# Kernel optimization log

Measured on AMD Instinct MI355X. Metric: run time of the kernel, lower is better.

## Reference

```python
import jax, jax.numpy as jnp
import numpy as np

D_MODEL = 1024
NUM_TILES = 8
BATCH = 4096
TEMPERATURE = 0.5

gelu = lambda x: jax.nn.gelu(x, approximate=False)  # torch nn.GELU default = exact erf


def setup_inputs() -> dict:
    key = jax.random.key(0)
    ks = jax.random.split(key, 12)
    d, t = D_MODEL, NUM_TILES
    s = lambda fan_in: 1.0 / np.sqrt(fan_in)
    return {
        "x": jax.random.normal(ks[0], (BATCH, d), jnp.float32),
        # router: Linear(d,d) -> GELU -> Linear(d,num_tiles); weights stored (in,out)
        "Wr1": jax.random.uniform(ks[1], (d, d), jnp.float32, -s(d), s(d)),
        "br1": jax.random.uniform(ks[2], (d,), jnp.float32, -s(d), s(d)),
        "Wr2": jax.random.uniform(ks[3], (d, t), jnp.float32, -s(d), s(d)),
        "br2": jax.random.uniform(ks[4], (t,), jnp.float32, -s(d), s(d)),
        # tile nets: Linear(d,2d) -> GELU -> Linear(2d,d), stacked over tiles
        "W1": jax.random.uniform(ks[5], (t, d, 2 * d), jnp.float32, -s(d), s(d)),
        "b1": jax.random.uniform(ks[6], (t, 2 * d), jnp.float32, -s(d), s(d)),
        "W2": jax.random.uniform(ks[7], (t, 2 * d, d), jnp.float32, -s(2 * d), s(2 * d)),
        "b2": jax.random.uniform(ks[8], (t, d), jnp.float32, -s(2 * d), s(2 * d)),
        # output projection Linear(d,d)
        "Wo": jax.random.uniform(ks[9], (d, d), jnp.float32, -s(d), s(d)),
        "bo": jax.random.uniform(ks[10], (d,), jnp.float32, -s(d), s(d)),
    }


def reference(x, Wr1, br1, Wr2, br2, W1, b1, W2, b2, Wo, bo):
    # router logits / temperature
    route_logits = (gelu(x @ Wr1 + br1) @ Wr2 + br2) / TEMPERATURE  # (B, T)
    tile_idx = jnp.argmax(route_logits, axis=-1)                    # (B,)

    # hard routing: compute all tile MLPs, then select the argmax tile per token
    # (dense equivalent of per-sample dispatch; same math as the torch loop)
    h = gelu(jnp.einsum("bd,tdf->btf", x, W1) + b1[None])           # (B, T, 2d)
    tile_out = jnp.einsum("btf,tfd->btd", h, W2) + b2[None]         # (B, T, d)
    selected = jnp.take_along_axis(tile_out, tile_idx[:, None, None], axis=1)[:, 0]  # (B, d)

    output = selected @ Wo + bo                                     # (B, d)
    return output, tile_idx, route_logits
```

## Files before the change

### kernel.cpp

```cpp
#include <hip/hip_runtime.h>
#include <hip/hip_bf16.h>
#include <math.h>
#include <stdint.h>

typedef __bf16 bf16_t;
typedef __bf16 bf16x8 __attribute__((ext_vector_type(8)));
typedef float  f32x4  __attribute__((ext_vector_type(4)));

#define BATCH   4096
#define DM      1024
#define DFF     2048
#define NTILES  8
#define MAXXB   40

__device__ __forceinline__ float gelu_exact(float x) {
    return 0.5f * x * (1.0f + erff(x * 0.70710678118654752440f));
}

__device__ __forceinline__ void async_ld16(const bf16_t* g, bf16_t* l) {
    __builtin_amdgcn_global_load_lds(
        (const __attribute__((address_space(1))) void*)g,
        (__attribute__((address_space(3))) void*)l, 16, 0, 0);
}

__device__ __forceinline__ f32x4 mfma16(bf16x8 a, bf16x8 b, f32x4 c) {
    return __builtin_amdgcn_mfma_f32_16x16x32_bf16(a, b, c, 0, 0, 0);
}

template<bool LO>
__device__ void tconv64_body(const float* __restrict__ src, bf16_t* __restrict__ outh,
                             bf16_t* __restrict__ outl, int K, int N, int kt, int nt,
                             float4* t , int tid) {
    const int k0 = kt * 64, n0 = nt * 64;
#pragma unroll
    for (int p = 0; p < 4; ++p) {
        int row = p * 16 + (tid >> 4);
        int c = tid & 15;
        float4 v = *(const float4*)(src + (size_t)(k0 + row) * N + n0 + c * 4);
        t[row * 16 + (c ^ ((row >> 2) & 15))] = v;
    }
    __syncthreads();
    const int n = tid >> 2, b = tid & 3;
    const float* tf = (const float*)t;
    float v[16];
#pragma unroll
    for (int i = 0; i < 16; ++i) {
        int k = 16 * b + i;
        int f4 = k * 16 + ((n >> 2) ^ ((k >> 2) & 15));
        v[i] = tf[f4 * 4 + (n & 3)];
    }
    bf16x8 h0, h1;
#pragma unroll
    for (int i = 0; i < 8; ++i) { h0[i] = (bf16_t)v[i]; h1[i] = (bf16_t)v[8 + i]; }
    size_t oi = (size_t)(n0 + n) * K + k0 + 16 * b;
    *(bf16x8*)(outh + oi) = h0;
    *(bf16x8*)(outh + oi + 8) = h1;
    if constexpr (LO) {
        bf16x8 l0, l1;
#pragma unroll
        for (int i = 0; i < 8; ++i) {
            l0[i] = (bf16_t)(v[i] - (float)h0[i]);
            l1[i] = (bf16_t)(v[8 + i] - (float)h1[i]);
        }
        *(bf16x8*)(outl + oi) = l0;
        *(bf16x8*)(outl + oi + 8) = l1;
    }
}

#define NCVT2 2048
#define PREP_A_GRID (NCVT2 + 256)

__global__ __launch_bounds__(256) void prep_a_kernel(
    const float* __restrict__ x, const float* __restrict__ Wr1,
    bf16_t* __restrict__ xh, bf16_t* __restrict__ xl,
    bf16_t* __restrict__ Wr1h, bf16_t* __restrict__ Wr1l) {
    __shared__ float4 t[64 * 16];
    int b = blockIdx.x;
    if (b < NCVT2) {
        size_t i = (size_t)b * 256 + threadIdx.x;
        const float4* x4 = (const float4*)x;
        float4 v0 = x4[2 * i], v1 = x4[2 * i + 1];
        float f[8] = {v0.x, v0.y, v0.z, v0.w, v1.x, v1.y, v1.z, v1.w};
        bf16x8 h, l;
#pragma unroll
        for (int j = 0; j < 8; ++j) { h[j] = (bf16_t)f[j]; l[j] = (bf16_t)(f[j] - (float)h[j]); }
        *(bf16x8*)(xh + i * 8) = h;
        *(bf16x8*)(xl + i * 8) = l;
        return;
    }
    b -= NCVT2;
    tconv64_body<true>(Wr1, Wr1h, Wr1l, DM, DM, b >> 4, b & 15, t, threadIdx.x);
}

template<bool SPLIT, bool GATHER, bool GELU, bool SCATTER, bool OUTF32, int BK>
__device__ __forceinline__ void gemm_body(
    const bf16_t* __restrict__ A, const bf16_t* __restrict__ Alo,
    const bf16_t* __restrict__ Bt, const bf16_t* __restrict__ Btlo,
    const float* __restrict__ bias,
    float* __restrict__ outF, bf16_t* __restrict__ outB,
    const int* __restrict__ perm, const int* __restrict__ counts,
    int M, int N, int K, int bx, int by,
    bf16_t* As, bf16_t* Bs, bf16_t* Asl, bf16_t* Bsl) {
    constexpr int NCH = BK / 32;
    constexpr int CH  = 128 * 32;
    constexpr int BUF = NCH * CH;

    int tile = 0, rb, cnt = M;
    const int* permT = nullptr;
    if constexpr (GATHER) {
        int xb = bx, t = 0, c = 0;
        while (t < NTILES) {
            c = counts[t];
            int nbk = (c + 127) >> 7;
            if (xb < nbk) break;
            xb -= nbk; ++t;
        }
        if (t == NTILES) return;
        tile = t;
        rb = xb * 128;
        cnt = c;
        permT = perm + tile * BATCH;
    } else {
        rb = bx * 128;
    }
    Bt   += (size_t)tile * K * N;
    if constexpr (SPLIT) Btlo += (size_t)tile * K * N;
    bias += (size_t)tile * N;

    const int lane = threadIdx.x & 63;
    const int wave = threadIdx.x >> 6;
    const int wm = wave & 1, wn = wave >> 1;
    const int nb = by * 128;

    const int srow = lane >> 2;
    const int scol = ((lane & 3) ^ (srow & 3)) * 8;
    const int row = wave * 16 + srow;
    int arow;
    if constexpr (GATHER) {
        int pos = rb + row;
        if (pos > cnt - 1) pos = cnt - 1;
        arow = permT[pos];
    } else {
        arow = rb + row;
    }
    const size_t aoff = (size_t)arow * K + scol;
    const size_t boff = (size_t)(nb + row) * K + scol;

    f32x4 acc[4][2];
#pragma unroll
    for (int i = 0; i < 4; ++i)
#pragma unroll
        for (int j = 0; j < 2; ++j) acc[i][j] = (f32x4){0.f, 0.f, 0.f, 0.f};

    const int lr = lane & 15, lq = lane >> 4;
    const int rdoff = (lr * 4 + (lq ^ (lr & 3))) * 8;

    auto stage = [&](int k0, int buf) {
#pragma unroll
        for (int c = 0; c < NCH; ++c) {
            async_ld16(A  + aoff + k0 + c * 32, &As[buf * BUF + c * CH + wave * 512]);
            async_ld16(Bt + boff + k0 + c * 32, &Bs[buf * BUF + c * CH + wave * 512]);
            if constexpr (SPLIT) {
                async_ld16(Alo  + aoff + k0 + c * 32, &Asl[buf * BUF + c * CH + wave * 512]);
                async_ld16(Btlo + boff + k0 + c * 32, &Bsl[buf * BUF + c * CH + wave * 512]);
            }
        }
    };

    auto compute = [&](int cur) {
#pragma unroll
        for (int kk = 0; kk < NCH; ++kk) {
            const int base = cur * BUF + kk * CH;
            bf16x8 af[4], bfr[2], afl[4], bfl[2];
#pragma unroll
            for (int i = 0; i < 4; ++i) {
                af[i] = *(const bf16x8*)&As[base + (wm * 4 + i) * 512 + rdoff];
                if constexpr (SPLIT)
                    afl[i] = *(const bf16x8*)&Asl[base + (wm * 4 + i) * 512 + rdoff];
            }
#pragma unroll
            for (int j = 0; j < 2; ++j) {
                bfr[j] = *(const bf16x8*)&Bs[base + (wn * 2 + j) * 512 + rdoff];
                if constexpr (SPLIT)
                    bfl[j] = *(const bf16x8*)&Bsl[base + (wn * 2 + j) * 512 + rdoff];
            }
#pragma unroll
            for (int i = 0; i < 4; ++i)
#pragma unroll
                for (int j = 0; j < 2; ++j) {
                    acc[i][j] = mfma16(af[i], bfr[j], acc[i][j]);
                    if constexpr (SPLIT) {
                        acc[i][j] = mfma16(af[i], bfl[j], acc[i][j]);
                        acc[i][j] = mfma16(afl[i], bfr[j], acc[i][j]);
                    }
                }
        }
    };

    stage(0, 0);
    int cur = 0;
    for (int k0 = 0; k0 < K; k0 += BK, cur ^= 1) {
        __syncthreads();
        if (k0 + BK < K) stage(k0 + BK, cur ^ 1);
        compute(cur);
    }

#pragma unroll
    for (int i = 0; i < 4; ++i) {
#pragma unroll
        for (int j = 0; j < 2; ++j) {
#pragma unroll
            for (int r = 0; r < 4; ++r) {
                int m = wm * 64 + i * 16 + lq * 4 + r;
                int n = wn * 32 + j * 16 + lr;
                int pos = rb + m;
                if constexpr (GATHER) { if (pos >= cnt) continue; }
                int grow;
                if constexpr (SCATTER) grow = permT[pos];
                else                   grow = pos;
                int gn = nb + n;
                float v = acc[i][j][r] + bias[gn];
                if constexpr (GELU) v = gelu_exact(v);
                if constexpr (OUTF32) outF[(size_t)grow * N + gn] = v;
                else                  outB[(size_t)grow * N + gn] = (bf16_t)v;
            }
        }
    }
}

#define NTCONV_TILES (4096 + 4096 + 256)
#define R1F_GRID (256 + NTCONV_TILES / 2)

__global__ __launch_bounds__(512) void r1_fused_kernel(
    const bf16_t* __restrict__ xh, const bf16_t* __restrict__ xl,
    const bf16_t* __restrict__ Wr1h, const bf16_t* __restrict__ Wr1l,
    const float* __restrict__ br1, float* __restrict__ Hr,
    const float* __restrict__ W1, const float* __restrict__ W2,
    const float* __restrict__ Wo,
    bf16_t* __restrict__ W1t, bf16_t* __restrict__ W2t, bf16_t* __restrict__ Wot) {
    __shared__ __align__(16) bf16_t smem[32768];
    const int bid = blockIdx.x;
    if (bid < 256) {
        gemm_body<true, false, true, false, true, 32>(
            xh, xl, Wr1h, Wr1l, br1, Hr, nullptr, nullptr, nullptr,
            BATCH, DM, DM, bid & 31, bid >> 5,
            smem, smem + 8192, smem + 16384, smem + 24576);
        return;
    }
    const int tix = bid - 256;
    const int half = threadIdx.x >> 8;
    const int tid = threadIdx.x & 255;
    float4* t = (float4*)smem + half * 1024;
    const int tile = tix * 2 + half;
    if (tile < 4096) {
        int mat = tile >> 9, r = tile & 511;
        size_t off = (size_t)mat * DM * DFF;
        tconv64_body<false>(W1 + off, W1t + off, nullptr, DM, DFF, r >> 5, r & 31, t, tid);
    } else if (tile < 8192) {
        int tt = tile - 4096;
        int mat = tt >> 9, r = tt & 511;
        size_t off = (size_t)mat * DM * DFF;
        tconv64_body<false>(W2 + off, W2t + off, nullptr, DFF, DM, r >> 4, r & 15, t, tid);
    } else {
        int r = tile - 8192;
        tconv64_body<false>(Wo, Wot, nullptr, DM, DM, r >> 4, r & 15, t, tid);
    }
}

template<bool GATHER, bool GELU, bool SCATTER, bool OUTF32>
__global__ __launch_bounds__(512) void gemm_ks_kernel(
    const bf16_t* __restrict__ A, const bf16_t* __restrict__ Bt,
    const float* __restrict__ bias,
    float* __restrict__ outF, bf16_t* __restrict__ outB,
    const int* __restrict__ perm, const int* __restrict__ counts,
    int M, int N, int K) {
    constexpr int CH  = 128 * 32;
    constexpr int BUF = 2 * CH;
    __shared__ __align__(16) bf16_t As[2 * BUF];
    __shared__ __align__(16) bf16_t Bs[2 * BUF];

    int tile = 0, rb, cnt = M;
    const int* permT = nullptr;
    if constexpr (GATHER) {
        int xb = blockIdx.x, t = 0, c = 0;
        while (t < NTILES) {
            c = counts[t];
            int nbk = (c + 127) >> 7;
            if (xb < nbk) break;
            xb -= nbk; ++t;
        }
        if (t == NTILES) return;
        tile = t;
        rb = xb * 128;
        cnt = c;
        permT = perm + tile * BATCH;
    } else {
        rb = blockIdx.x * 128;
    }
    Bt   += (size_t)tile * K * N;
    bias += (size_t)tile * N;

    const int lane = threadIdx.x & 63;
    const int wave = threadIdx.x >> 6;
    const int wm = wave & 1, wn = (wave >> 1) & 1;
    const int h  = wave >> 2;
    const int nb = blockIdx.y * 128;

    const int srow = lane >> 2;
    const int scol = ((lane & 3) ^ (srow & 3)) * 8;
    const int row = wave * 16 + srow;
    int arow;
    if constexpr (GATHER) {
        int pos = rb + row;
        if (pos > cnt - 1) pos = cnt - 1;
        arow = permT[pos];
    } else {
        arow = rb + row;
    }
    const size_t aoff = (size_t)arow * K + scol;
    const size_t boff = (size_t)(nb + row) * K + scol;

    f32x4 acc[4][4];
#pragma unroll
    for (int i = 0; i < 4; ++i)
#pragma unroll
        for (int j = 0; j < 4; ++j) acc[i][j] = (f32x4){0.f, 0.f, 0.f, 0.f};

    const int lr = lane & 15, lq = lane >> 4;
    const int rdoff = (lr * 4 + (lq ^ (lr & 3))) * 8;

    auto stage = [&](int k0, int buf) {
#pragma unroll
        for (int c = 0; c < 2; ++c) {
            async_ld16(A  + aoff + k0 + c * 32, &As[buf * BUF + c * CH + wave * 512]);
            async_ld16(Bt + boff + k0 + c * 32, &Bs[buf * BUF + c * CH + wave * 512]);
        }
    };

    stage(0, 0);
    int cur = 0;
    for (int k0 = 0; k0 < K; k0 += 64, cur ^= 1) {
        __syncthreads();
        if (k0 + 64 < K) stage(k0 + 64, cur ^ 1);
        const int base = cur * BUF + h * CH;
        bf16x8 af[4], bf[4];
#pragma unroll
        for (int i = 0; i < 4; ++i)
            af[i] = *(const bf16x8*)&As[base + (wm * 4 + i) * 512 + rdoff];
#pragma unroll
        for (int j = 0; j < 4; ++j)
            bf[j] = *(const bf16x8*)&Bs[base + (wn * 4 + j) * 512 + rdoff];
#pragma unroll
        for (int i = 0; i < 4; ++i)
#pragma unroll
            for (int j = 0; j < 4; ++j)
                acc[i][j] = mfma16(af[i], bf[j], acc[i][j]);
    }

    __syncthreads();
    const int region = wn * 2 + wm;
    float* rbuf = ((region & 2) ? (float*)Bs : (float*)As) + (region & 1) * 4096;
    if (h == 1) {
#pragma unroll
        for (int i = 0; i < 4; ++i)
#pragma unroll
            for (int j = 0; j < 4; ++j)
                *(f32x4*)&rbuf[(i * 4 + j) * 256 + lane * 4] = acc[i][j];
    }
    __syncthreads();
    if (h == 1) return;
#pragma unroll
    for (int i = 0; i < 4; ++i)
#pragma unroll
        for (int j = 0; j < 4; ++j) {
            f32x4 p = *(const f32x4*)&rbuf[(i * 4 + j) * 256 + lane * 4];
            acc[i][j] += p;
        }

#pragma unroll
    for (int i = 0; i < 4; ++i) {
#pragma unroll
        for (int j = 0; j < 4; ++j) {
#pragma unroll
            for (int r = 0; r < 4; ++r) {
                int m = wm * 64 + i * 16 + lq * 4 + r;
                int n = wn * 64 + j * 16 + lr;
                int pos = rb + m;
                if constexpr (GATHER) { if (pos >= cnt) continue; }
                int grow;
                if constexpr (SCATTER) grow = permT[pos];
                else                   grow = pos;
                int gn = nb + n;
                float v = acc[i][j][r] + bias[gn];
                if constexpr (GELU) v = gelu_exact(v);
                if constexpr (OUTF32) outF[(size_t)grow * N + gn] = v;
                else                  outB[(size_t)grow * N + gn] = (bf16_t)v;
            }
        }
    }
}

__global__ __launch_bounds__(256) void router2_kernel(
    const float* __restrict__ Hr, const float* __restrict__ Wr2, const float* __restrict__ br2,
    float* __restrict__ outLog, float* __restrict__ outIdx,
    int* __restrict__ counts, int* __restrict__ perm) {
    __shared__ float w2s[DM * 9];
    __shared__ int h[NTILES], base[NTILES];
    const int tid = threadIdx.x;
    if (tid < NTILES) h[tid] = 0;
    for (int e = tid; e < DM * 8; e += 256) {
        int k = e >> 3, j = e & 7;
        w2s[k * 9 + j] = Wr2[e];
    }
    __syncthreads();

    const int lane = tid & 63, wave = tid >> 6;
    const int sub = lane >> 4;
    const int lr16 = lane & 15;
    const int row = blockIdx.x * 16 + wave * 4 + sub;

    const float4* Hr4 = (const float4*)Hr;
    float acc[8];
#pragma unroll
    for (int j = 0; j < 8; ++j) acc[j] = 0.f;

#pragma unroll
    for (int i = 0; i < 16; ++i) {
        int f = lr16 + i * 16;
        float4 hv = Hr4[(size_t)row * 256 + f];
        float hx[4] = {hv.x, hv.y, hv.z, hv.w};
        int kbase = f * 4;
#pragma unroll
        for (int d = 0; d < 4; ++d) {
            float xv = hx[d];
            const float* w = &w2s[(kbase + d) * 9];
#pragma unroll
            for (int j = 0; j < 8; ++j) acc[j] += xv * w[j];
        }
    }
#pragma unroll
    for (int off = 8; off; off >>= 1)
#pragma unroll
        for (int j = 0; j < 8; ++j) acc[j] += __shfl_down(acc[j], off);

    int bi = 0, rank = 0;
    if (lr16 == 0) {
        float best = -1e30f;
        float lg[8];
#pragma unroll
        for (int j = 0; j < 8; ++j) {
            float v = (acc[j] + br2[j]) * 2.0f;
            lg[j] = v;
            if (v > best) { best = v; bi = j; }
        }
        float4 lo = {lg[0], lg[1], lg[2], lg[3]};
        float4 hi = {lg[4], lg[5], lg[6], lg[7]};
        *(float4*)(outLog + (size_t)row * 8)     = lo;
        *(float4*)(outLog + (size_t)row * 8 + 4) = hi;
        outIdx[row] = (float)bi;
        rank = atomicAdd(&h[bi], 1);
    }
    __syncthreads();
    if (tid < NTILES && h[tid] > 0) base[tid] = atomicAdd(&counts[tid], h[tid]);
    __syncthreads();
    if (lr16 == 0) perm[bi * BATCH + base[bi] + rank] = row;
}

extern "C" void kernel_launch(void* const* d_in, const int* in_sizes, int n_in,
                              void* d_out, int out_size, void* d_ws, size_t ws_size,
                              hipStream_t stream) {
    const float* x   = (const float*)d_in[0];
    const float* Wr1 = (const float*)d_in[1];
    const float* br1 = (const float*)d_in[2];
    const float* Wr2 = (const float*)d_in[3];
    const float* br2 = (const float*)d_in[4];
    const float* W1  = (const float*)d_in[5];
    const float* b1  = (const float*)d_in[6];
    const float* W2  = (const float*)d_in[7];
    const float* b2  = (const float*)d_in[8];
    const float* Wo  = (const float*)d_in[9];
    const float* bo  = (const float*)d_in[10];

    char* ws = (char*)d_ws;
    size_t o = 0;
    auto carve = [&](size_t bytes) { char* p = ws + o; o = (o + bytes + 255) & ~(size_t)255; return p; };
    bf16_t* Wr1h = (bf16_t*)carve((size_t)DM * DM * 2);
    bf16_t* Wr1l = (bf16_t*)carve((size_t)DM * DM * 2);
    bf16_t* Wot  = (bf16_t*)carve((size_t)DM * DM * 2);
    bf16_t* W1t  = (bf16_t*)carve((size_t)NTILES * DM * DFF * 2);
    bf16_t* W2t  = (bf16_t*)carve((size_t)NTILES * DM * DFF * 2);
    bf16_t* xh   = (bf16_t*)carve((size_t)BATCH * DM * 2);
    bf16_t* xl   = (bf16_t*)carve((size_t)BATCH * DM * 2);
    bf16_t* H1   = (bf16_t*)carve((size_t)BATCH * DFF * 2);
    bf16_t* sel  = (bf16_t*)carve((size_t)BATCH * DM * 2);
    float*  Hr   = (float*)carve((size_t)BATCH * DM * 4);
    int*    counts = (int*)carve(NTILES * sizeof(int));
    int*    perm   = (int*)carve((size_t)NTILES * BATCH * sizeof(int));

    float* outMain = (float*)d_out;
    float* outIdx  = outMain + (size_t)BATCH * DM;
    float* outLog  = outIdx + BATCH;

    hipMemsetAsync(counts, 0, NTILES * sizeof(int), stream);

    prep_a_kernel<<<PREP_A_GRID, 256, 0, stream>>>(x, Wr1, xh, xl, Wr1h, Wr1l);

    r1_fused_kernel<<<R1F_GRID, 512, 0, stream>>>(xh, xl, Wr1h, Wr1l, br1, Hr,
                                                  W1, W2, Wo, W1t, W2t, Wot);

    router2_kernel<<<BATCH / 16, 256, 0, stream>>>(Hr, Wr2, br2, outLog, outIdx, counts, perm);

    gemm_ks_kernel<true, true, true, false><<<dim3(MAXXB, DFF / 128, 1), 512, 0, stream>>>(
        xh, W1t, b1, nullptr, H1, perm, counts, BATCH, DFF, DM);

    gemm_ks_kernel<true, false, true, false><<<dim3(MAXXB, DM / 128, 1), 512, 0, stream>>>(
        H1, W2t, b2, nullptr, sel, perm, counts, BATCH, DM, DFF);

    gemm_ks_kernel<false, false, false, true><<<dim3(BATCH / 128, DM / 128, 1), 512, 0, stream>>>(
        sel, Wot, bo, outMain, nullptr, nullptr, nullptr, BATCH, DM, DM);
}
```

Before: 390.5 us.

## Replace split-K 8-wave GEMM with 4-wave non-split GEMM kernel

```diff
diff --git a/kernel.cpp b/kernel.cpp
--- a/kernel.cpp
+++ b/kernel.cpp
@@ -268,14 +268,13 @@
 }
 
 template<bool GATHER, bool GELU, bool SCATTER, bool OUTF32>
-__global__ __launch_bounds__(512) void gemm_ks_kernel(
+__global__ __launch_bounds__(256) void gemm4w_kernel(
     const bf16_t* __restrict__ A, const bf16_t* __restrict__ Bt,
     const float* __restrict__ bias,
     float* __restrict__ outF, bf16_t* __restrict__ outB,
     const int* __restrict__ perm, const int* __restrict__ counts,
     int M, int N, int K) {
-    constexpr int CH  = 128 * 32;
-    constexpr int BUF = 2 * CH;
+    constexpr int BUF = 128 * 32;
     __shared__ __align__(16) bf16_t As[2 * BUF];
     __shared__ __align__(16) bf16_t Bs[2 * BUF];
 
@@ -302,23 +301,27 @@
 
     const int lane = threadIdx.x & 63;
     const int wave = threadIdx.x >> 6;
-    const int wm = wave & 1, wn = (wave >> 1) & 1;
-    const int h  = wave >> 2;
+    const int wm = wave & 1, wn = wave >> 1;
     const int nb = blockIdx.y * 128;
 
     const int srow = lane >> 2;
     const int scol = ((lane & 3) ^ (srow & 3)) * 8;
-    const int row = wave * 16 + srow;
-    int arow;
-    if constexpr (GATHER) {
-        int pos = rb + row;
-        if (pos > cnt - 1) pos = cnt - 1;
-        arow = permT[pos];
-    } else {
-        arow = rb + row;
-    }
-    const size_t aoff = (size_t)arow * K + scol;
-    const size_t boff = (size_t)(nb + row) * K + scol;
+    size_t aoff[2], boff[2];
+#pragma unroll
+    for (int r = 0; r < 2; ++r) {
+        int seg = r * 4 + wave;
+        int row = seg * 16 + srow;
+        int arow;
+        if constexpr (GATHER) {
+            int pos = rb + row;
+            if (pos > cnt - 1) pos = cnt - 1;
+            arow = permT[pos];
+        } else {
+            arow = rb + row;
+        }
+        aoff[r] = (size_t)arow * K + scol;
+        boff[r] = (size_t)(nb + row) * K + scol;
+    }
 
     f32x4 acc[4][4];
 #pragma unroll
@@ -331,51 +334,31 @@
 
     auto stage = [&](int k0, int buf) {
 #pragma unroll
-        for (int c = 0; c < 2; ++c) {
-            async_ld16(A  + aoff + k0 + c * 32, &As[buf * BUF + c * CH + wave * 512]);
-            async_ld16(Bt + boff + k0 + c * 32, &Bs[buf * BUF + c * CH + wave * 512]);
+        for (int r = 0; r < 2; ++r) {
+            int seg = r * 4 + wave;
+            async_ld16(A  + aoff[r] + k0, &As[buf * BUF + seg * 512]);
+            async_ld16(Bt + boff[r] + k0, &Bs[buf * BUF + seg * 512]);
         }
     };
 
     stage(0, 0);
     int cur = 0;
-    for (int k0 = 0; k0 < K; k0 += 64, cur ^= 1) {
+    for (int k0 = 0; k0 < K; k0 += 32, cur ^= 1) {
         __syncthreads();
-        if (k0 + 64 < K) stage(k0 + 64, cur ^ 1);
-        const int base = cur * BUF + h * CH;
+        if (k0 + 32 < K) stage(k0 + 32, cur ^ 1);
         bf16x8 af[4], bf[4];
 #pragma unroll
         for (int i = 0; i < 4; ++i)
-            af[i] = *(const bf16x8*)&As[base + (wm * 4 + i) * 512 + rdoff];
+            af[i] = *(const bf16x8*)&As[cur * BUF + (wm * 4 + i) * 512 + rdoff];
 #pragma unroll
         for (int j = 0; j < 4; ++j)
-            bf[j] = *(const bf16x8*)&Bs[base + (wn * 4 + j) * 512 + rdoff];
+            bf[j] = *(const bf16x8*)&Bs[cur * BUF + (wn * 4 + j) * 512 + rdoff];
 #pragma unroll
         for (int i = 0; i < 4; ++i)
 #pragma unroll
             for (int j = 0; j < 4; ++j)
                 acc[i][j] = mfma16(af[i], bf[j], acc[i][j]);
     }
-
-    __syncthreads();
-    const int region = wn * 2 + wm;
-    float* rbuf = ((region & 2) ? (float*)Bs : (float*)As) + (region & 1) * 4096;
-    if (h == 1) {
-#pragma unroll
-        for (int i = 0; i < 4; ++i)
-#pragma unroll
-            for (int j = 0; j < 4; ++j)
-                *(f32x4*)&rbuf[(i * 4 + j) * 256 + lane * 4] = acc[i][j];
-    }
-    __syncthreads();
-    if (h == 1) return;
-#pragma unroll
-    for (int i = 0; i < 4; ++i)
-#pragma unroll
-        for (int j = 0; j < 4; ++j) {
-            f32x4 p = *(const f32x4*)&rbuf[(i * 4 + j) * 256 + lane * 4];
-            acc[i][j] += p;
-        }
 
 #pragma unroll
     for (int i = 0; i < 4; ++i) {
@@ -510,12 +493,12 @@
 
     router2_kernel<<<BATCH / 16, 256, 0, stream>>>(Hr, Wr2, br2, outLog, outIdx, counts, perm);
 
-    gemm_ks_kernel<true, true, true, false><<<dim3(MAXXB, DFF / 128, 1), 512, 0, stream>>>(
+    gemm4w_kernel<true, true, true, false><<<dim3(MAXXB, DFF / 128, 1), 256, 0, stream>>>(
         xh, W1t, b1, nullptr, H1, perm, counts, BATCH, DFF, DM);
 
-    gemm_ks_kernel<true, false, true, false><<<dim3(MAXXB, DM / 128, 1), 512, 0, stream>>>(
+    gemm4w_kernel<true, false, true, false><<<dim3(MAXXB, DM / 128, 1), 256, 0, stream>>>(
         H1, W2t, b2, nullptr, sel, perm, counts, BATCH, DM, DFF);
 
-    gemm_ks_kernel<false, false, false, true><<<dim3(BATCH / 128, DM / 128, 1), 512, 0, stream>>>(
+    gemm4w_kernel<false, false, false, true><<<dim3(BATCH / 128, DM / 128, 1), 256, 0, stream>>>(
         sel, Wot, bo, outMain, nullptr, nullptr, nullptr, BATCH, DM, DM);
 }
```

Measured after the change: 351.8 us. 1.11x faster.
